# Kernel tuning notes

Hardware: AMD Instinct MI355X
Metric: run time of the kernel (lower is better)

## Reference

```python
import jax, jax.numpy as jnp
import numpy as np

B, S, D, H = 16, 1024, 512, 8
HD = D // H  # head dim = 64
NEG_INF = jnp.float32(-jnp.inf)


def setup_inputs() -> dict:
    key = jax.random.key(0)
    ks = jax.random.split(key, 7)
    s = 0.02
    return {
        "Q": jax.random.normal(ks[0], (B, S, D), dtype=jnp.float32),
        "Wq_w": jax.random.normal(ks[1], (D, D), dtype=jnp.float32) * s,
        "Wq_b": jax.random.normal(ks[2], (D,), dtype=jnp.float32) * s,
        "Wk_w": jax.random.normal(ks[3], (D, D), dtype=jnp.float32) * s,
        "Wk_b": jax.random.normal(ks[4], (D,), dtype=jnp.float32) * s,
        "Wv_w": jax.random.normal(ks[5], (D, D), dtype=jnp.float32) * s,
        "Wv_b": jax.random.normal(ks[6], (D,), dtype=jnp.float32) * s,
        "ln_w": jnp.ones((D,), dtype=jnp.float32),
        "ln_b": jnp.zeros((D,), dtype=jnp.float32),
    }


def _heads(x):  # [B,S,D] -> [B,H,S,HD]
    return x.reshape(B, S, H, HD).transpose(0, 2, 1, 3)


def reference(Q, Wq_w, Wq_b, Wk_w, Wk_b, Wv_w, Wv_b, ln_w, ln_b):
    # row mask: a row is padding iff all features are zero; True in attn_mask = masked
    valid = jnp.any(Q != 0, axis=-1)                      # [B,S]
    attn_mask = ~(valid[:, :, None] & valid[:, None, :])  # [B,S,S], True=masked
    add_mask = jnp.where(attn_mask, NEG_INF, 0.0)[:, None, :, :]  # [B,1,S,S]

    q = jax.nn.relu(Q @ Wq_w.T + Wq_b)
    k = jax.nn.relu(Q @ Wk_w.T + Wk_b)
    v = jax.nn.relu(Q @ Wv_w.T + Wv_b)
    qh, kh, vh = _heads(q), _heads(k), _heads(v)          # [B,H,S,HD]

    scale = 1.0 / np.sqrt(HD)
    scores = jnp.einsum("bhqd,bhkd->bhqk", qh, kh) * scale + add_mask
    w = jax.nn.softmax(scores, axis=-1)
    w = jnp.nan_to_num(w, nan=0.0)  # fully-masked rows -> 0 (matches torch nan_to_num)
    # dropout p=0.0 (eval) -> identity
    attn = jnp.einsum("bhqk,bhkd->bhqd", w, vh)

    out = attn + qh                                       # residual in multiheaded view
    out = out.transpose(0, 2, 1, 3).reshape(B, S, D)      # from_multiheaded

    mu = jnp.mean(out, axis=-1, keepdims=True)
    var = jnp.var(out, axis=-1, keepdims=True)
    out = (out - mu) * jax.lax.rsqrt(var + 1e-5) * ln_w + ln_b
    out = jax.nn.relu(out)

    weights = w.reshape(B * H, S, S)  # matches torch [B*H, S, S]
    return out, weights
```

## Files before the change

### kernel.cpp

```cpp
#include <hip/hip_runtime.h>
#include <stdint.h>

typedef unsigned short u16;
typedef __attribute__((ext_vector_type(8))) __bf16 bf16x8;
typedef __attribute__((ext_vector_type(4))) float f32x4;

__device__ __forceinline__ u16 f2bf(float f) {
    unsigned u = __float_as_uint(f);
    u += 0x7fffu + ((u >> 16) & 1u);
    return (u16)(u >> 16);
}
__device__ __forceinline__ float bf2f(u16 h) {
    return __uint_as_float(((unsigned)h) << 16);
}

__global__ void k_prep(const float* __restrict__ Q,
                       const float* __restrict__ Wq, const float* __restrict__ Wk,
                       const float* __restrict__ Wv,
                       u16* __restrict__ qb, u16* __restrict__ wall,
                       float* __restrict__ fmask) {
    int bid = blockIdx.x;
    int t = threadIdx.x;
    if (bid < 16384) {
        const float* src = Q + (size_t)bid * 512;
        u16* dst = qb + (size_t)bid * 512;
        float4 v0 = *(const float4*)(src + t * 4);
        float4 v1 = *(const float4*)(src + 256 + t * 4);
        bool nz = (v0.x != 0.f) || (v0.y != 0.f) || (v0.z != 0.f) || (v0.w != 0.f) ||
                  (v1.x != 0.f) || (v1.y != 0.f) || (v1.z != 0.f) || (v1.w != 0.f);
        ushort4 o0 = make_ushort4(f2bf(v0.x), f2bf(v0.y), f2bf(v0.z), f2bf(v0.w));
        ushort4 o1 = make_ushort4(f2bf(v1.x), f2bf(v1.y), f2bf(v1.z), f2bf(v1.w));
        *(ushort4*)(dst + t * 4) = o0;
        *(ushort4*)(dst + 256 + t * 4) = o1;
        unsigned long long bal = __ballot(nz);
        if (t == 0) fmask[bid] = bal ? 0.0f : -1e30f;
    } else {
        int r = bid - 16384;
        const float* W = (r < 512) ? Wq : (r < 1024) ? Wk : Wv;
        const float* src = W + (size_t)(r & 511) * 512;
        u16* dst = wall + (size_t)r * 512;
        float4 v0 = *(const float4*)(src + t * 4);
        float4 v1 = *(const float4*)(src + 256 + t * 4);
        ushort4 o0 = make_ushort4(f2bf(v0.x), f2bf(v0.y), f2bf(v0.z), f2bf(v0.w));
        ushort4 o1 = make_ushort4(f2bf(v1.x), f2bf(v1.y), f2bf(v1.z), f2bf(v1.w));
        *(ushort4*)(dst + t * 4) = o0;
        *(ushort4*)(dst + 256 + t * 4) = o1;
    }
}

__global__ __launch_bounds__(256) void k_qkv(
        const u16* __restrict__ qb, const u16* __restrict__ wall,
        const float* __restrict__ bq, const float* __restrict__ bk,
        const float* __restrict__ bv,
        u16* __restrict__ oq, u16* __restrict__ ok, u16* __restrict__ ov) {
    __shared__ u16 As[128 * 32];
    __shared__ u16 Bs[128 * 32];
    int bm = blockIdx.x, bn = blockIdx.y;
    int tid = threadIdx.x, lane = tid & 63, wid = tid >> 6;
    int wm = wid >> 1, wn = wid & 1;
    int q4 = lane >> 4, l16 = lane & 15;

    f32x4 acc[4][4];
#pragma unroll
    for (int i = 0; i < 4; ++i)
#pragma unroll
        for (int j = 0; j < 4; ++j) acc[i][j] = (f32x4){0.f, 0.f, 0.f, 0.f};

#pragma unroll 1
    for (int kk = 0; kk < 16; ++kk) {
        float4 av[2], bw[2];
#pragma unroll
        for (int c = 0; c < 2; ++c) {
            int id = c * 256 + tid;
            int r = id >> 2, cb = (id & 3) * 8;
            av[c] = *(const float4*)(qb + ((size_t)(bm * 128 + r)) * 512 + kk * 32 + cb);
            bw[c] = *(const float4*)(wall + ((size_t)(bn * 128 + r)) * 512 + kk * 32 + cb);
        }
        __syncthreads();
#pragma unroll
        for (int c = 0; c < 2; ++c) {
            int id = c * 256 + tid;
            int r = id >> 2, cb = (id & 3) * 8;
            *(float4*)(&As[r * 32 + cb]) = av[c];
            *(float4*)(&Bs[r * 32 + cb]) = bw[c];
        }
        __syncthreads();
        bf16x8 af[4], bf[4];
#pragma unroll
        for (int i = 0; i < 4; ++i)
            af[i] = *(const bf16x8*)(&As[(wm * 64 + i * 16 + l16) * 32 + q4 * 8]);
#pragma unroll
        for (int j = 0; j < 4; ++j)
            bf[j] = *(const bf16x8*)(&Bs[(wn * 64 + j * 16 + l16) * 32 + q4 * 8]);
#pragma unroll
        for (int i = 0; i < 4; ++i)
#pragma unroll
            for (int j = 0; j < 4; ++j)
                acc[i][j] = __builtin_amdgcn_mfma_f32_16x16x32_bf16(af[i], bf[j], acc[i][j], 0, 0, 0);
    }

    int which = bn >> 2;
    const float* bias = (which == 0) ? bq : (which == 1) ? bk : bv;
    u16* outp = (which == 0) ? oq : (which == 1) ? ok : ov;
#pragma unroll
    for (int i = 0; i < 4; ++i)
#pragma unroll
        for (int j = 0; j < 4; ++j) {
            int n = bn * 128 + wn * 64 + j * 16 + l16;
            int c = n & 511;
            float bb = bias[c];
#pragma unroll
            for (int r = 0; r < 4; ++r) {
                int m = bm * 128 + wm * 64 + i * 16 + q4 * 4 + r;
                float val = acc[i][j][r] + bb;
                val = fmaxf(val, 0.f);
                outp[(size_t)m * 512 + c] = f2bf(val);
            }
        }
}

__global__ void k_vt(const u16* __restrict__ v, u16* __restrict__ vT) {
    __shared__ u16 tile[32][33];
    int bmRow = blockIdx.x;
    int bc = blockIdx.y;
    int tx = threadIdx.x & 31, ty = threadIdx.x >> 5;
#pragma unroll
    for (int q = 0; q < 4; ++q) {
        int ml = ty + q * 8;
        tile[ml][tx] = v[((size_t)(bmRow * 32 + ml)) * 512 + bc * 32 + tx];
    }
    __syncthreads();
    int b = bmRow >> 5;
    int sbase = (bmRow & 31) * 32;
#pragma unroll
    for (int q = 0; q < 4; ++q) {
        int cl = ty + q * 8;
        vT[((size_t)(b * 512 + bc * 32 + cl)) * 1024 + sbase + tx] = tile[tx][cl];
    }
}

__global__ __launch_bounds__(256, 2) void k_attn(
        const u16* __restrict__ qv, const u16* __restrict__ kv,
        const u16* __restrict__ vT, const float* __restrict__ fmask,
        float* __restrict__ outAtt, float* __restrict__ outW) {
    __shared__ u16 Qs[64 * 72];
    __shared__ u16 Ks[128 * 72];
    __shared__ u16 Vs[64 * 136];
    __shared__ u16 Ws[4 * 16 * 136];
    __shared__ float kmf[128];

    int bid = blockIdx.x;
    int qt = bid & 15, h = (bid >> 4) & 7, b = bid >> 7;
    int tid = threadIdx.x, lane = tid & 63, w = tid >> 6;
    int q4 = lane >> 4, l16 = lane & 15;
    const float scale = 0.125f;

    size_t qrow0 = (size_t)b * 1024 + qt * 64;
    size_t headcol = (size_t)h * 64;

#pragma unroll
    for (int c = 0; c < 2; ++c) {
        int id = c * 256 + tid;
        int r = id >> 3, cb = (id & 7) * 8;
        float4 t4 = *(const float4*)(qv + (qrow0 + r) * 512 + headcol + cb);
        *(float4*)(&Qs[r * 72 + cb]) = t4;
    }

    float qmv[4], mrun[4], lrun[4];
#pragma unroll
    for (int r = 0; r < 4; ++r) {
        qmv[r] = fmask[qrow0 + w * 16 + q4 * 4 + r];
        mrun[r] = -3e38f;
        lrun[r] = 0.f;
    }

    for (int kt = 0; kt < 8; ++kt) {
        __syncthreads();
        size_t krow0 = (size_t)b * 1024 + kt * 128;
#pragma unroll
        for (int c = 0; c < 4; ++c) {
            int id = c * 256 + tid;
            int r = id >> 3, cb = (id & 7) * 8;
            float4 t4 = *(const float4*)(kv + (krow0 + r) * 512 + headcol + cb);
            *(float4*)(&Ks[r * 72 + cb]) = t4;
        }
        if (tid < 128) kmf[tid] = fmask[krow0 + tid];
        __syncthreads();

        bf16x8 a0 = *(const bf16x8*)(&Qs[(w * 16 + l16) * 72 + q4 * 8]);
        bf16x8 a1 = *(const bf16x8*)(&Qs[(w * 16 + l16) * 72 + 32 + q4 * 8]);
        float km[8];
#pragma unroll
        for (int j = 0; j < 8; ++j) km[j] = kmf[j * 16 + l16];
        f32x4 acc[8];
#pragma unroll
        for (int j = 0; j < 8; ++j) acc[j] = (f32x4){0.f, 0.f, 0.f, 0.f};
#pragma unroll
        for (int j = 0; j < 8; ++j) {
            bf16x8 b0 = *(const bf16x8*)(&Ks[(j * 16 + l16) * 72 + q4 * 8]);
            bf16x8 b1 = *(const bf16x8*)(&Ks[(j * 16 + l16) * 72 + 32 + q4 * 8]);
            acc[j] = __builtin_amdgcn_mfma_f32_16x16x32_bf16(a0, b0, acc[j], 0, 0, 0);
            acc[j] = __builtin_amdgcn_mfma_f32_16x16x32_bf16(a1, b1, acc[j], 0, 0, 0);
        }
#pragma unroll
        for (int r = 0; r < 4; ++r) {
            float mt = -3e38f;
#pragma unroll
            for (int j = 0; j < 8; ++j) {
                float s = acc[j][r] * scale + qmv[r] + km[j];
                acc[j][r] = s;
                mt = fmaxf(mt, s);
            }
#pragma unroll
            for (int mm = 1; mm <= 8; mm <<= 1) mt = fmaxf(mt, __shfl_xor(mt, mm, 64));
            float mnew = fmaxf(mrun[r], mt);
            float ps = 0.f;
#pragma unroll
            for (int j = 0; j < 8; ++j) ps += __expf(acc[j][r] - mnew);
#pragma unroll
            for (int mm = 1; mm <= 8; mm <<= 1) ps += __shfl_xor(ps, mm, 64);
            lrun[r] = lrun[r] * __expf(mrun[r] - mnew) + ps;
            mrun[r] = mnew;
        }
    }
    float rl[4];
#pragma unroll
    for (int r = 0; r < 4; ++r)
        rl[r] = (qmv[r] == 0.f) ? (1.f / lrun[r]) : 0.f;

    f32x4 accO[4];
#pragma unroll
    for (int jn = 0; jn < 4; ++jn) accO[jn] = (f32x4){0.f, 0.f, 0.f, 0.f};
    size_t wbase = ((size_t)(b * 8 + h)) * 1024 * 1024;
    u16* wsw = &Ws[w * 16 * 136];

    for (int kt = 0; kt < 8; ++kt) {
        __syncthreads();
        size_t krow0 = (size_t)b * 1024 + kt * 128;
#pragma unroll
        for (int c = 0; c < 4; ++c) {
            int id = c * 256 + tid;
            int r = id >> 3, cb = (id & 7) * 8;
            float4 t4 = *(const float4*)(kv + (krow0 + r) * 512 + headcol + cb);
            *(float4*)(&Ks[r * 72 + cb]) = t4;
        }
#pragma unroll
        for (int c = 0; c < 4; ++c) {
            int id = c * 256 + tid;
            int hd = id >> 4, cb = (id & 15) * 8;
            float4 t4 = *(const float4*)(vT + ((size_t)(b * 512) + headcol + hd) * 1024 + kt * 128 + cb);
            *(float4*)(&Vs[hd * 136 + cb]) = t4;
        }
        if (tid < 128) kmf[tid] = fmask[krow0 + tid];
        __syncthreads();

        bf16x8 a0 = *(const bf16x8*)(&Qs[(w * 16 + l16) * 72 + q4 * 8]);
        bf16x8 a1 = *(const bf16x8*)(&Qs[(w * 16 + l16) * 72 + 32 + q4 * 8]);
        float km[8];
#pragma unroll
        for (int j = 0; j < 8; ++j) km[j] = kmf[j * 16 + l16];
        f32x4 acc[8];
#pragma unroll
        for (int j = 0; j < 8; ++j) acc[j] = (f32x4){0.f, 0.f, 0.f, 0.f};
#pragma unroll
        for (int j = 0; j < 8; ++j) {
            bf16x8 b0 = *(const bf16x8*)(&Ks[(j * 16 + l16) * 72 + q4 * 8]);
            bf16x8 b1 = *(const bf16x8*)(&Ks[(j * 16 + l16) * 72 + 32 + q4 * 8]);
            acc[j] = __builtin_amdgcn_mfma_f32_16x16x32_bf16(a0, b0, acc[j], 0, 0, 0);
            acc[j] = __builtin_amdgcn_mfma_f32_16x16x32_bf16(a1, b1, acc[j], 0, 0, 0);
        }
#pragma unroll
        for (int j = 0; j < 8; ++j) {
#pragma unroll
            for (int r = 0; r < 4; ++r) {
                int rowC = q4 * 4 + r;
                float s = acc[j][r] * scale + qmv[r] + km[j];
                float wv = __expf(s - mrun[r]) * rl[r];
                outW[wbase + (size_t)(qt * 64 + w * 16 + rowC) * 1024 + kt * 128 + j * 16 + l16] = wv;
                wsw[rowC * 136 + j * 16 + l16] = f2bf(wv);
            }
        }
#pragma unroll
        for (int ks = 0; ks < 4; ++ks) {
            bf16x8 aw = *(const bf16x8*)(&wsw[l16 * 136 + ks * 32 + q4 * 8]);
#pragma unroll
            for (int jn = 0; jn < 4; ++jn) {
                bf16x8 bv = *(const bf16x8*)(&Vs[(jn * 16 + l16) * 136 + ks * 32 + q4 * 8]);
                accO[jn] = __builtin_amdgcn_mfma_f32_16x16x32_bf16(aw, bv, accO[jn], 0, 0, 0);
            }
        }
    }

#pragma unroll
    for (int jn = 0; jn < 4; ++jn)
#pragma unroll
        for (int r = 0; r < 4; ++r) {
            int rowC = q4 * 4 + r;
            int hd = jn * 16 + l16;
            float qres = bf2f(Qs[(w * 16 + rowC) * 72 + hd]);
            float o = accO[jn][r] + qres;
            outAtt[(qrow0 + w * 16 + rowC) * 512 + headcol + hd] = o;
        }
}

__global__ void k_ln(float* __restrict__ io, const float* __restrict__ lw,
                     const float* __restrict__ lb) {
    int row = blockIdx.x;
    int t = threadIdx.x;
    float* p = io + (size_t)row * 512;
    float4 x0 = *(const float4*)(p + t * 4);
    float4 x1 = *(const float4*)(p + 256 + t * 4);
    float s = x0.x + x0.y + x0.z + x0.w + x1.x + x1.y + x1.z + x1.w;
    float s2 = x0.x * x0.x + x0.y * x0.y + x0.z * x0.z + x0.w * x0.w +
               x1.x * x1.x + x1.y * x1.y + x1.z * x1.z + x1.w * x1.w;
#pragma unroll
    for (int mm = 1; mm <= 32; mm <<= 1) {
        s += __shfl_xor(s, mm, 64);
        s2 += __shfl_xor(s2, mm, 64);
    }
    float mean = s * (1.f / 512.f);
    float var = s2 * (1.f / 512.f) - mean * mean;
    float inv = rsqrtf(var + 1e-5f);
    float4 w0 = *(const float4*)(lw + t * 4);
    float4 w1 = *(const float4*)(lw + 256 + t * 4);
    float4 b0 = *(const float4*)(lb + t * 4);
    float4 b1 = *(const float4*)(lb + 256 + t * 4);
    float4 o0, o1;
    o0.x = fmaxf((x0.x - mean) * inv * w0.x + b0.x, 0.f);
    o0.y = fmaxf((x0.y - mean) * inv * w0.y + b0.y, 0.f);
    o0.z = fmaxf((x0.z - mean) * inv * w0.z + b0.z, 0.f);
    o0.w = fmaxf((x0.w - mean) * inv * w0.w + b0.w, 0.f);
    o1.x = fmaxf((x1.x - mean) * inv * w1.x + b1.x, 0.f);
    o1.y = fmaxf((x1.y - mean) * inv * w1.y + b1.y, 0.f);
    o1.z = fmaxf((x1.z - mean) * inv * w1.z + b1.z, 0.f);
    o1.w = fmaxf((x1.w - mean) * inv * w1.w + b1.w, 0.f);
    *(float4*)(p + t * 4) = o0;
    *(float4*)(p + 256 + t * 4) = o1;
}

extern "C" void kernel_launch(void* const* d_in, const int* in_sizes, int n_in,
                              void* d_out, int out_size, void* d_ws, size_t ws_size,
                              hipStream_t stream) {
    const float* Q = (const float*)d_in[0];
    const float* Wq_w = (const float*)d_in[1];
    const float* Wq_b = (const float*)d_in[2];
    const float* Wk_w = (const float*)d_in[3];
    const float* Wk_b = (const float*)d_in[4];
    const float* Wv_w = (const float*)d_in[5];
    const float* Wv_b = (const float*)d_in[6];
    const float* ln_w = (const float*)d_in[7];
    const float* ln_b = (const float*)d_in[8];

    u16* ws16 = (u16*)d_ws;
    u16* qb   = ws16;
    u16* wall = ws16 + 8388608;
    u16* oq   = ws16 + 9175040;
    u16* okk  = ws16 + 17563648;
    u16* ov   = ws16 + 25952256;
    u16* vT   = ws16 + 34340864;
    float* fmask = (float*)((char*)d_ws + 85458944);

    float* outAtt = (float*)d_out;
    float* outW = (float*)d_out + 8388608;

    k_prep<<<17920, 64, 0, stream>>>(Q, Wq_w, Wk_w, Wv_w, qb, wall, fmask);
    k_qkv<<<dim3(128, 12), 256, 0, stream>>>(qb, wall, Wq_b, Wk_b, Wv_b, oq, okk, ov);
    k_vt<<<dim3(512, 16), 256, 0, stream>>>(ov, vT);
    k_attn<<<2048, 256, 0, stream>>>(oq, okk, vT, fmask, outAtt, outW);
    k_ln<<<16384, 64, 0, stream>>>(outAtt, ln_w, ln_b);
}
```

Measured before the change: 869.0 us.

## Single-pass attention with LDS-resident weights and fused V transpose

Merges the two-pass softmax into one pass. Unnormalized exp scores for the full key range are kept in 160KB of dynamic LDS, and the attention output and weights are normalized at the end; the running max is dropped. The separate V transpose kernel is removed by having the QKV GEMM epilogue write V transposed directly. LDS tiles use an XOR swizzle, and occupancy drops to one block per CU. Omitting max subtraction risks overflow if scores grow large.

```diff
diff --git a/kernel.cpp b/kernel.cpp
--- a/kernel.cpp
+++ b/kernel.cpp
@@ -3,6 +3,7 @@
 
 typedef unsigned short u16;
 typedef __attribute__((ext_vector_type(8))) __bf16 bf16x8;
+typedef __attribute__((ext_vector_type(8))) u16 u16x8;
 typedef __attribute__((ext_vector_type(4))) float f32x4;
 
 __device__ __forceinline__ u16 f2bf(float f) {
@@ -52,7 +53,7 @@
         const u16* __restrict__ qb, const u16* __restrict__ wall,
         const float* __restrict__ bq, const float* __restrict__ bk,
         const float* __restrict__ bv,
-        u16* __restrict__ oq, u16* __restrict__ ok, u16* __restrict__ ov) {
+        u16* __restrict__ oq, u16* __restrict__ ok, u16* __restrict__ vT) {
     __shared__ u16 As[128 * 32];
     __shared__ u16 Bs[128 * 32];
     int bm = blockIdx.x, bn = blockIdx.y;
@@ -100,54 +101,53 @@
     }
 
     int which = bn >> 2;
-    const float* bias = (which == 0) ? bq : (which == 1) ? bk : bv;
-    u16* outp = (which == 0) ? oq : (which == 1) ? ok : ov;
-#pragma unroll
-    for (int i = 0; i < 4; ++i)
-#pragma unroll
-        for (int j = 0; j < 4; ++j) {
-            int n = bn * 128 + wn * 64 + j * 16 + l16;
-            int c = n & 511;
-            float bb = bias[c];
-#pragma unroll
-            for (int r = 0; r < 4; ++r) {
-                int m = bm * 128 + wm * 64 + i * 16 + q4 * 4 + r;
-                float val = acc[i][j][r] + bb;
-                val = fmaxf(val, 0.f);
-                outp[(size_t)m * 512 + c] = f2bf(val);
+    if (which < 2) {
+        const float* bias = (which == 0) ? bq : bk;
+        u16* outp = (which == 0) ? oq : ok;
+#pragma unroll
+        for (int i = 0; i < 4; ++i)
+#pragma unroll
+            for (int j = 0; j < 4; ++j) {
+                int n = bn * 128 + wn * 64 + j * 16 + l16;
+                int c = n & 511;
+                float bb = bias[c];
+#pragma unroll
+                for (int r = 0; r < 4; ++r) {
+                    int m = bm * 128 + wm * 64 + i * 16 + q4 * 4 + r;
+                    float val = acc[i][j][r] + bb;
+                    val = fmaxf(val, 0.f);
+                    outp[(size_t)m * 512 + c] = f2bf(val);
+                }
             }
-        }
-}
-
-__global__ void k_vt(const u16* __restrict__ v, u16* __restrict__ vT) {
-    __shared__ u16 tile[32][33];
-    int bmRow = blockIdx.x;
-    int bc = blockIdx.y;
-    int tx = threadIdx.x & 31, ty = threadIdx.x >> 5;
-#pragma unroll
-    for (int q = 0; q < 4; ++q) {
-        int ml = ty + q * 8;
-        tile[ml][tx] = v[((size_t)(bmRow * 32 + ml)) * 512 + bc * 32 + tx];
-    }
-    __syncthreads();
-    int b = bmRow >> 5;
-    int sbase = (bmRow & 31) * 32;
-#pragma unroll
-    for (int q = 0; q < 4; ++q) {
-        int cl = ty + q * 8;
-        vT[((size_t)(b * 512 + bc * 32 + cl)) * 1024 + sbase + tx] = tile[tx][cl];
-    }
-}
-
-__global__ __launch_bounds__(256, 2) void k_attn(
+    } else {
+        size_t vrow0 = (size_t)(bm >> 3) * 512;
+        int s0base = ((bm & 7) * 128) + wm * 64;
+#pragma unroll
+        for (int i = 0; i < 4; ++i)
+#pragma unroll
+            for (int j = 0; j < 4; ++j) {
+                int c = (bn * 128 + wn * 64 + j * 16 + l16) & 511;
+                float bb = bv[c];
+                ushort4 o;
+                o.x = f2bf(fmaxf(acc[i][j][0] + bb, 0.f));
+                o.y = f2bf(fmaxf(acc[i][j][1] + bb, 0.f));
+                o.z = f2bf(fmaxf(acc[i][j][2] + bb, 0.f));
+                o.w = f2bf(fmaxf(acc[i][j][3] + bb, 0.f));
+                int s0 = s0base + i * 16 + q4 * 4;
+                *(ushort4*)(vT + (vrow0 + c) * 1024 + s0) = o;
+            }
+    }
+}
+
+__global__ __launch_bounds__(256, 1) void k_attn(
         const u16* __restrict__ qv, const u16* __restrict__ kv,
         const u16* __restrict__ vT, const float* __restrict__ fmask,
         float* __restrict__ outAtt, float* __restrict__ outW) {
-    __shared__ u16 Qs[64 * 72];
-    __shared__ u16 Ks[128 * 72];
-    __shared__ u16 Vs[64 * 136];
-    __shared__ u16 Ws[4 * 16 * 136];
-    __shared__ float kmf[128];
+    extern __shared__ char smem[];
+    char* Wsb = smem;
+    char* Ksb = smem + 131072;
+    char* Vsb = smem + 147456;
+    float* linv = (float*)(smem + 131072);
 
     int bid = blockIdx.x;
     int qt = bid & 15, h = (bid >> 4) & 7, b = bid >> 7;
@@ -158,149 +158,131 @@
     size_t qrow0 = (size_t)b * 1024 + qt * 64;
     size_t headcol = (size_t)h * 64;
 
-#pragma unroll
-    for (int c = 0; c < 2; ++c) {
-        int id = c * 256 + tid;
-        int r = id >> 3, cb = (id & 7) * 8;
-        float4 t4 = *(const float4*)(qv + (qrow0 + r) * 512 + headcol + cb);
-        *(float4*)(&Qs[r * 72 + cb]) = t4;
-    }
-
-    float qmv[4], mrun[4], lrun[4];
+    const u16* qp = qv + (qrow0 + w * 16 + l16) * 512 + headcol;
+    bf16x8 a0 = *(const bf16x8*)(qp + q4 * 8);
+    bf16x8 a1 = *(const bf16x8*)(qp + 32 + q4 * 8);
+
+    float qmv[4], lrun[4];
 #pragma unroll
     for (int r = 0; r < 4; ++r) {
         qmv[r] = fmask[qrow0 + w * 16 + q4 * 4 + r];
-        mrun[r] = -3e38f;
         lrun[r] = 0.f;
     }
-
+    f32x4 accO[4];
+#pragma unroll
+    for (int jn = 0; jn < 4; ++jn) accO[jn] = (f32x4){0.f, 0.f, 0.f, 0.f};
+
+#pragma unroll 1
     for (int kt = 0; kt < 8; ++kt) {
+        size_t krow0 = (size_t)b * 1024 + kt * 128;
         __syncthreads();
-        size_t krow0 = (size_t)b * 1024 + kt * 128;
 #pragma unroll
         for (int c = 0; c < 4; ++c) {
             int id = c * 256 + tid;
             int r = id >> 3, cb = (id & 7) * 8;
             float4 t4 = *(const float4*)(kv + (krow0 + r) * 512 + headcol + cb);
-            *(float4*)(&Ks[r * 72 + cb]) = t4;
-        }
-        if (tid < 128) kmf[tid] = fmask[krow0 + tid];
-        __syncthreads();
-
-        bf16x8 a0 = *(const bf16x8*)(&Qs[(w * 16 + l16) * 72 + q4 * 8]);
-        bf16x8 a1 = *(const bf16x8*)(&Qs[(w * 16 + l16) * 72 + 32 + q4 * 8]);
-        float km[8];
-#pragma unroll
-        for (int j = 0; j < 8; ++j) km[j] = kmf[j * 16 + l16];
-        f32x4 acc[8];
-#pragma unroll
-        for (int j = 0; j < 8; ++j) acc[j] = (f32x4){0.f, 0.f, 0.f, 0.f};
-#pragma unroll
-        for (int j = 0; j < 8; ++j) {
-            bf16x8 b0 = *(const bf16x8*)(&Ks[(j * 16 + l16) * 72 + q4 * 8]);
-            bf16x8 b1 = *(const bf16x8*)(&Ks[(j * 16 + l16) * 72 + 32 + q4 * 8]);
-            acc[j] = __builtin_amdgcn_mfma_f32_16x16x32_bf16(a0, b0, acc[j], 0, 0, 0);
-            acc[j] = __builtin_amdgcn_mfma_f32_16x16x32_bf16(a1, b1, acc[j], 0, 0, 0);
-        }
-#pragma unroll
-        for (int r = 0; r < 4; ++r) {
-            float mt = -3e38f;
-#pragma unroll
-            for (int j = 0; j < 8; ++j) {
-                float s = acc[j][r] * scale + qmv[r] + km[j];
-                acc[j][r] = s;
-                mt = fmaxf(mt, s);
-            }
-#pragma unroll
-            for (int mm = 1; mm <= 8; mm <<= 1) mt = fmaxf(mt, __shfl_xor(mt, mm, 64));
-            float mnew = fmaxf(mrun[r], mt);
-            float ps = 0.f;
-#pragma unroll
-            for (int j = 0; j < 8; ++j) ps += __expf(acc[j][r] - mnew);
-#pragma unroll
-            for (int mm = 1; mm <= 8; mm <<= 1) ps += __shfl_xor(ps, mm, 64);
-            lrun[r] = lrun[r] * __expf(mrun[r] - mnew) + ps;
-            mrun[r] = mnew;
-        }
-    }
-    float rl[4];
-#pragma unroll
-    for (int r = 0; r < 4; ++r)
-        rl[r] = (qmv[r] == 0.f) ? (1.f / lrun[r]) : 0.f;
-
-    f32x4 accO[4];
-#pragma unroll
-    for (int jn = 0; jn < 4; ++jn) accO[jn] = (f32x4){0.f, 0.f, 0.f, 0.f};
-    size_t wbase = ((size_t)(b * 8 + h)) * 1024 * 1024;
-    u16* wsw = &Ws[w * 16 * 136];
-
-    for (int kt = 0; kt < 8; ++kt) {
-        __syncthreads();
-        size_t krow0 = (size_t)b * 1024 + kt * 128;
-#pragma unroll
-        for (int c = 0; c < 4; ++c) {
-            int id = c * 256 + tid;
-            int r = id >> 3, cb = (id & 7) * 8;
-            float4 t4 = *(const float4*)(kv + (krow0 + r) * 512 + headcol + cb);
-            *(float4*)(&Ks[r * 72 + cb]) = t4;
+            *(float4*)(Ksb + ((r * 128 + cb * 2) ^ ((r & 7) << 4))) = t4;
         }
 #pragma unroll
         for (int c = 0; c < 4; ++c) {
             int id = c * 256 + tid;
             int hd = id >> 4, cb = (id & 15) * 8;
-            float4 t4 = *(const float4*)(vT + ((size_t)(b * 512) + headcol + hd) * 1024 + kt * 128 + cb);
-            *(float4*)(&Vs[hd * 136 + cb]) = t4;
-        }
-        if (tid < 128) kmf[tid] = fmask[krow0 + tid];
+            float4 t4 = *(const float4*)(vT + ((size_t)b * 512 + headcol + hd) * 1024 + kt * 128 + cb);
+            *(float4*)(Vsb + ((hd * 256 + cb * 2) ^ ((hd & 7) << 4))) = t4;
+        }
+        float km[8];
+#pragma unroll
+        for (int j = 0; j < 8; ++j) km[j] = fmask[krow0 + j * 16 + l16];
         __syncthreads();
 
-        bf16x8 a0 = *(const bf16x8*)(&Qs[(w * 16 + l16) * 72 + q4 * 8]);
-        bf16x8 a1 = *(const bf16x8*)(&Qs[(w * 16 + l16) * 72 + 32 + q4 * 8]);
-        float km[8];
-#pragma unroll
-        for (int j = 0; j < 8; ++j) km[j] = kmf[j * 16 + l16];
         f32x4 acc[8];
 #pragma unroll
         for (int j = 0; j < 8; ++j) acc[j] = (f32x4){0.f, 0.f, 0.f, 0.f};
 #pragma unroll
         for (int j = 0; j < 8; ++j) {
-            bf16x8 b0 = *(const bf16x8*)(&Ks[(j * 16 + l16) * 72 + q4 * 8]);
-            bf16x8 b1 = *(const bf16x8*)(&Ks[(j * 16 + l16) * 72 + 32 + q4 * 8]);
+            int kr = j * 16 + l16;
+            bf16x8 b0 = *(const bf16x8*)(Ksb + ((kr * 128 + q4 * 16) ^ ((kr & 7) << 4)));
+            bf16x8 b1 = *(const bf16x8*)(Ksb + ((kr * 128 + 64 + q4 * 16) ^ ((kr & 7) << 4)));
             acc[j] = __builtin_amdgcn_mfma_f32_16x16x32_bf16(a0, b0, acc[j], 0, 0, 0);
             acc[j] = __builtin_amdgcn_mfma_f32_16x16x32_bf16(a1, b1, acc[j], 0, 0, 0);
         }
 #pragma unroll
-        for (int j = 0; j < 8; ++j) {
+        for (int j = 0; j < 8; ++j)
+#pragma unroll
+            for (int r = 0; r < 4; ++r)
+                acc[j][r] = __expf(acc[j][r] * scale + qmv[r] + km[j]);
+#pragma unroll
+        for (int r = 0; r < 4; ++r) {
+            float ps = 0.f;
+#pragma unroll
+            for (int j = 0; j < 8; ++j) ps += acc[j][r];
+#pragma unroll
+            for (int mm = 1; mm <= 8; mm <<= 1) ps += __shfl_xor(ps, mm, 64);
+            lrun[r] += ps;
+        }
+        int wrbase = w * 16 + q4 * 4;
+#pragma unroll
+        for (int j = 0; j < 8; ++j)
 #pragma unroll
             for (int r = 0; r < 4; ++r) {
-                int rowC = q4 * 4 + r;
-                float s = acc[j][r] * scale + qmv[r] + km[j];
-                float wv = __expf(s - mrun[r]) * rl[r];
-                outW[wbase + (size_t)(qt * 64 + w * 16 + rowC) * 1024 + kt * 128 + j * 16 + l16] = wv;
-                wsw[rowC * 136 + j * 16 + l16] = f2bf(wv);
+                int row = wrbase + r;
+                int boff = (row * 2048 + kt * 256 + j * 32 + l16 * 2) ^ ((row & 7) << 4);
+                *(u16*)(Wsb + boff) = f2bf(acc[j][r]);
             }
-        }
+        int arow = w * 16 + l16;
 #pragma unroll
         for (int ks = 0; ks < 4; ++ks) {
-            bf16x8 aw = *(const bf16x8*)(&wsw[l16 * 136 + ks * 32 + q4 * 8]);
+            bf16x8 aw = *(const bf16x8*)(Wsb + ((arow * 2048 + kt * 256 + ks * 64 + q4 * 16) ^ ((arow & 7) << 4)));
 #pragma unroll
             for (int jn = 0; jn < 4; ++jn) {
-                bf16x8 bv = *(const bf16x8*)(&Vs[(jn * 16 + l16) * 136 + ks * 32 + q4 * 8]);
-                accO[jn] = __builtin_amdgcn_mfma_f32_16x16x32_bf16(aw, bv, accO[jn], 0, 0, 0);
+                int vrow = jn * 16 + l16;
+                bf16x8 bvv = *(const bf16x8*)(Vsb + ((vrow * 256 + ks * 64 + q4 * 16) ^ ((vrow & 7) << 4)));
+                accO[jn] = __builtin_amdgcn_mfma_f32_16x16x32_bf16(aw, bvv, accO[jn], 0, 0, 0);
             }
         }
     }
 
+    float rl[4];
+#pragma unroll
+    for (int r = 0; r < 4; ++r)
+        rl[r] = (qmv[r] == 0.f && lrun[r] > 0.f) ? (1.f / lrun[r]) : 0.f;
+
+    __syncthreads();
+    if (l16 == 0) {
+#pragma unroll
+        for (int r = 0; r < 4; ++r) linv[w * 16 + q4 * 4 + r] = rl[r];
+    }
+
 #pragma unroll
     for (int jn = 0; jn < 4; ++jn)
 #pragma unroll
         for (int r = 0; r < 4; ++r) {
-            int rowC = q4 * 4 + r;
+            int rowC = w * 16 + q4 * 4 + r;
             int hd = jn * 16 + l16;
-            float qres = bf2f(Qs[(w * 16 + rowC) * 72 + hd]);
-            float o = accO[jn][r] + qres;
-            outAtt[(qrow0 + w * 16 + rowC) * 512 + headcol + hd] = o;
-        }
+            float qres = bf2f(qv[(qrow0 + rowC) * 512 + headcol + hd]);
+            outAtt[(qrow0 + rowC) * 512 + headcol + hd] = accO[jn][r] * rl[r] + qres;
+        }
+    __syncthreads();
+
+    int row = tid >> 2, cq = tid & 3;
+    float rlr = linv[row];
+    size_t wbase = (((size_t)(b * 8 + h)) * 1024 + qt * 64 + row) * 1024;
+#pragma unroll 4
+    for (int ch = 0; ch < 32; ++ch) {
+        int col = ch * 32 + cq * 8;
+        u16x8 wv = *(const u16x8*)(Wsb + ((row * 2048 + col * 2) ^ ((row & 7) << 4)));
+        float4 o0, o1;
+        o0.x = bf2f(wv[0]) * rlr;
+        o0.y = bf2f(wv[1]) * rlr;
+        o0.z = bf2f(wv[2]) * rlr;
+        o0.w = bf2f(wv[3]) * rlr;
+        o1.x = bf2f(wv[4]) * rlr;
+        o1.y = bf2f(wv[5]) * rlr;
+        o1.z = bf2f(wv[6]) * rlr;
+        o1.w = bf2f(wv[7]) * rlr;
+        *(float4*)(outW + wbase + col) = o0;
+        *(float4*)(outW + wbase + col + 4) = o1;
+    }
 }
 
 __global__ void k_ln(float* __restrict__ io, const float* __restrict__ lw,
@@ -356,16 +338,21 @@
     u16* wall = ws16 + 8388608;
     u16* oq   = ws16 + 9175040;
     u16* okk  = ws16 + 17563648;
-    u16* ov   = ws16 + 25952256;
-    u16* vT   = ws16 + 34340864;
-    float* fmask = (float*)((char*)d_ws + 85458944);
+    u16* vT   = ws16 + 25952256;
+    float* fmask = (float*)((char*)d_ws + 68681728);
 
     float* outAtt = (float*)d_out;
     float* outW = (float*)d_out + 8388608;
 
+    static bool s_attr = false;
+    if (!s_attr) {
+        hipFuncSetAttribute((const void*)k_attn,
+                            hipFuncAttributeMaxDynamicSharedMemorySize, 163840);
+        s_attr = true;
+    }
+
     k_prep<<<17920, 64, 0, stream>>>(Q, Wq_w, Wk_w, Wv_w, qb, wall, fmask);
-    k_qkv<<<dim3(128, 12), 256, 0, stream>>>(qb, wall, Wq_b, Wk_b, Wv_b, oq, okk, ov);
-    k_vt<<<dim3(512, 16), 256, 0, stream>>>(ov, vT);
-    k_attn<<<2048, 256, 0, stream>>>(oq, okk, vT, fmask, outAtt, outW);
+    k_qkv<<<dim3(128, 12), 256, 0, stream>>>(qb, wall, Wq_b, Wk_b, Wv_b, oq, okk, vT);
+    k_attn<<<2048, 256, 163840, stream>>>(oq, okk, vT, fmask, outAtt, outW);
     k_ln<<<16384, 64, 0, stream>>>(outAtt, ln_w, ln_b);
 }
```

Result: no change. 883.1 us (+1.6%).
